# Performance work log

Measured on AMD Instinct MI355X. Metric: run time of the kernel, lower is better.

## Reference

```python
import jax, jax.numpy as jnp
import numpy as np

IN_F = 4096
OUT_F = 4096
B, S = 4, 2048


def _quantize_weight(w_float):
    """Replicates Int4PackedLinear.__init__ double quantization; returns reg_b and w_scale."""
    w_amax = jnp.abs(w_float).max()
    scale = jnp.where(w_amax == 0, 1.0, w_amax / 127.0)
    w_int8 = jnp.clip(jnp.round(w_float / scale), -127, 127).astype(jnp.int8)
    low4_amax = jnp.abs(w_int8.astype(jnp.float32)).max()
    low4_scale = jnp.where(low4_amax == 0, 1.0, low4_amax / 7.0)
    w_low = jnp.clip(jnp.round(w_int8.astype(jnp.float32) / low4_scale), -7, 7).astype(jnp.int8)
    w_rec = jnp.round(w_low.astype(jnp.float32) * low4_scale).astype(jnp.int8)
    w_high = jnp.clip(w_int8.astype(jnp.int32) - w_rec.astype(jnp.int32), -7, 7).astype(jnp.int8)
    reg_b = (w_rec.astype(jnp.int32) + w_high.astype(jnp.int32)).astype(jnp.int8)  # w_combined
    return reg_b, scale.astype(jnp.float32)


def setup_inputs() -> dict:
    key = jax.random.key(0)
    k1, k2, k3 = jax.random.split(key, 3)
    w_float = jax.random.normal(k1, (OUT_F, IN_F), dtype=jnp.float32) * 0.02
    reg_b, w_scale = _quantize_weight(w_float)
    x = jax.random.normal(k2, (B, S, IN_F), dtype=jnp.float32)
    bias = jax.random.normal(k3, (OUT_F,), dtype=jnp.float32) * 0.01
    # gate=1.0 >= threshold=0.3 -> full-precision INT8 path uses reg_b
    return {"x": x, "w_int": reg_b, "w_scale": w_scale, "bias": bias}


def reference(x, w_int, w_scale, bias):
    # --- dynamic per-tensor activation quantization ---
    x_amax = jnp.abs(x).max()
    x_scale = jnp.where(x_amax == 0, jnp.float32(1.0), x_amax / 127.0)
    x_int8 = jnp.clip(jnp.round(x / x_scale), -127, 127).astype(jnp.int8)
    # --- integer matmul (accumulate in int32, like torch._int_mm) ---
    out_i32 = jnp.einsum(
        'bsk,nk->bsn',
        x_int8.astype(jnp.int32),
        w_int.astype(jnp.int32),
    )  # [B, S, OUT_F]
    # --- dequant scale in bf16 AFTER the integer matmul, then bias add ---
    combined_scale = (x_scale * w_scale).astype(jnp.bfloat16)
    out = out_i32.astype(jnp.bfloat16) * combined_scale
    out = out + bias  # bf16 + fp32 -> fp32, matching torch promotion
    return out
```

## Files before the change

kernel.cpp:

```cpp
#include <hip/hip_runtime.h>
#include <hip/hip_bf16.h>
#include <stdint.h>

#define IN_F  4096
#define OUT_F 4096
#define BSZ   4
#define SEQ   2048
#define MDIM  (BSZ * SEQ)

typedef __attribute__((address_space(1))) uint8_t ga_u8_t;
typedef __attribute__((address_space(3))) uint8_t ls_u8_t;

__device__ __forceinline__ void gload16_lds(const void* g, void* l) {
    __builtin_amdgcn_global_load_lds((ga_u8_t*)g, (ls_u8_t*)l, 16, 0, 0);
}

__device__ __forceinline__ float bf16_rne(float f) {
    unsigned u = __float_as_uint(f);
    u = (u + 0x7fffu + ((u >> 16) & 1u)) & 0xffff0000u;
    return __uint_as_float(u);
}

__global__ void amax_kernel(const float* __restrict__ x, int n4,
                            unsigned int* __restrict__ amax_u) {
    const float4* x4 = (const float4*)x;
    int idx = blockIdx.x * blockDim.x + threadIdx.x;
    int stride = gridDim.x * blockDim.x;
    float m = 0.0f;
    for (int i = idx; i < n4; i += stride) {
        float4 v = x4[i];
        m = fmaxf(m, fmaxf(fmaxf(fabsf(v.x), fabsf(v.y)),
                           fmaxf(fabsf(v.z), fabsf(v.w))));
    }
    for (int off = 32; off > 0; off >>= 1)
        m = fmaxf(m, __shfl_down(m, off, 64));
    __shared__ float sm[4];
    int lane = threadIdx.x & 63, wave = threadIdx.x >> 6;
    if (lane == 0) sm[wave] = m;
    __syncthreads();
    if (threadIdx.x == 0) {
        m = fmaxf(fmaxf(sm[0], sm[1]), fmaxf(sm[2], sm[3]));
        atomicMax(amax_u, __float_as_uint(m));
    }
}

__global__ void quant_kernel(const float* __restrict__ x,
                             signed char* __restrict__ x8,
                             const unsigned int* __restrict__ amax_u, int n4) {
    float amax = __uint_as_float(*amax_u);
    float xs = (amax == 0.0f) ? 1.0f : (amax / 127.0f);
    int idx = blockIdx.x * blockDim.x + threadIdx.x;
    if (idx < n4) {
        float4 v = ((const float4*)x)[idx];
        char4 q;
        q.x = (signed char)fminf(fmaxf(rintf(v.x / xs), -127.0f), 127.0f);
        q.y = (signed char)fminf(fmaxf(rintf(v.y / xs), -127.0f), 127.0f);
        q.z = (signed char)fminf(fmaxf(rintf(v.z / xs), -127.0f), 127.0f);
        q.w = (signed char)fminf(fmaxf(rintf(v.w / xs), -127.0f), 127.0f);
        ((char4*)x8)[idx] = q;
    }
}

__global__ void convw_kernel(const int* __restrict__ w,
                             signed char* __restrict__ w8, int n4) {
    int idx = blockIdx.x * blockDim.x + threadIdx.x;
    if (idx < n4) {
        int4 v = ((const int4*)w)[idx];
        char4 q;
        q.x = (signed char)v.x; q.y = (signed char)v.y;
        q.z = (signed char)v.z; q.w = (signed char)v.w;
        ((char4*)w8)[idx] = q;
    }
}

__global__ __launch_bounds__(256, 2) void gemm_i8_kernel(
    const signed char* __restrict__ A,
    const signed char* __restrict__ B,
    const unsigned int* __restrict__ amax_u,
    const float* __restrict__ wscale_p,
    const float* __restrict__ bias,
    float* __restrict__ out) {
    __shared__ signed char sA[128 * 64];
    __shared__ signed char sB[128 * 64];

    const int t = threadIdx.x;
    const int lane = t & 63;
    const int wave = t >> 6;
    const int wm = wave >> 1;
    const int wn = wave & 1;
    const int tileM = blockIdx.y * 128;
    const int tileN = blockIdx.x * 128;

    const int g0 = t, g1 = t + 256;
    const int ar0 = g0 >> 2, ac0 = ((g0 & 3) ^ ((ar0 >> 1) & 3)) * 16;
    const int ar1 = g1 >> 2, ac1 = ((g1 & 3) ^ ((ar1 >> 1) & 3)) * 16;

    const signed char* gA0 = A + (size_t)(tileM + ar0) * IN_F + ac0;
    const signed char* gA1 = A + (size_t)(tileM + ar1) * IN_F + ac1;
    const signed char* gB0 = B + (size_t)(tileN + ar0) * IN_F + ac0;
    const signed char* gB1 = B + (size_t)(tileN + ar1) * IN_F + ac1;

    signed char* lA0 = sA + g0 * 16;
    signed char* lA1 = sA + g1 * 16;
    signed char* lB0 = sB + g0 * 16;
    signed char* lB1 = sB + g1 * 16;

    using i32x4 = __attribute__((ext_vector_type(4))) int;
    i32x4 acc[4][4] = {};

    const signed char* aptr[4];
    const signed char* bptr[4];
#pragma unroll
    for (int i = 0; i < 4; ++i) {
        int rowa = wm * 64 + i * 16 + (lane & 15);
        int ca = ((lane >> 4) ^ ((rowa >> 1) & 3)) * 16;
        aptr[i] = sA + rowa * 64 + ca;
        int rowb = wn * 64 + i * 16 + (lane & 15);
        int cb = ((lane >> 4) ^ ((rowb >> 1) & 3)) * 16;
        bptr[i] = sB + rowb * 64 + cb;
    }

    for (int k0 = 0; k0 < IN_F; k0 += 64) {
        __syncthreads();
        gload16_lds(gA0 + k0, lA0);
        gload16_lds(gA1 + k0, lA1);
        gload16_lds(gB0 + k0, lB0);
        gload16_lds(gB1 + k0, lB1);
        __syncthreads();

        i32x4 aF[4], bF[4];
#pragma unroll
        for (int i = 0; i < 4; ++i) aF[i] = *(const i32x4*)aptr[i];
#pragma unroll
        for (int j = 0; j < 4; ++j) bF[j] = *(const i32x4*)bptr[j];
#pragma unroll
        for (int i = 0; i < 4; ++i)
#pragma unroll
            for (int j = 0; j < 4; ++j)
                acc[i][j] = __builtin_amdgcn_mfma_i32_16x16x64_i8(
                    aF[i], bF[j], acc[i][j], 0, 0, 0);
    }

    float amax = __uint_as_float(*amax_u);
    float xs = (amax == 0.0f) ? 1.0f : (amax / 127.0f);
    float cs = bf16_rne(xs * wscale_p[0]);

#pragma unroll
    for (int j = 0; j < 4; ++j) {
        int n = tileN + wn * 64 + j * 16 + (lane & 15);
        float bz = bias[n];
#pragma unroll
        for (int i = 0; i < 4; ++i) {
            int row0 = tileM + wm * 64 + i * 16 + (lane >> 4) * 4;
#pragma unroll
            for (int r = 0; r < 4; ++r) {
                float v = bf16_rne((float)acc[i][j][r]);
                float p = bf16_rne(v * cs);
                out[(size_t)(row0 + r) * OUT_F + n] = p + bz;
            }
        }
    }
}

extern "C" void kernel_launch(void* const* d_in, const int* in_sizes, int n_in,
                              void* d_out, int out_size, void* d_ws,
                              size_t ws_size, hipStream_t stream) {
    const float* x = (const float*)d_in[0];
    const int* w_int = (const int*)d_in[1];
    const float* w_scale = (const float*)d_in[2];
    const float* bias = (const float*)d_in[3];
    float* out = (float*)d_out;

    unsigned char* ws = (unsigned char*)d_ws;
    unsigned int* amax_u = (unsigned int*)ws;
    signed char* w8 = (signed char*)(ws + 64);
    signed char* x8 = (signed char*)(ws + 64 + (size_t)OUT_F * IN_F);

    hipMemsetAsync(amax_u, 0, 4, stream);

    const int n_x = MDIM * IN_F;
    const int n_w = OUT_F * IN_F;

    amax_kernel<<<4096, 256, 0, stream>>>(x, n_x / 4, amax_u);
    quant_kernel<<<(n_x / 4) / 256, 256, 0, stream>>>(x, x8, amax_u, n_x / 4);
    convw_kernel<<<(n_w / 4) / 256, 256, 0, stream>>>(w_int, w8, n_w / 4);

    dim3 grid(OUT_F / 128, MDIM / 128);
    gemm_i8_kernel<<<grid, 256, 0, stream>>>(x8, w8, amax_u, w_scale, bias, out);
}
```

Baseline: 472.6 us.

## Use 32x32x32 int8 MFMA with 128-wide K tiles and fuse prep kernels

Switches the GEMM inner loop from 16x16x64 to 32x32x32 int8 MFMA instructions. The K tile doubles to 128, with a new LDS layout that groups 16-byte chunks by K-slice, and launch bounds rise to 4 blocks per CU. The activation-quantize and weight-convert kernels are merged into one launch to save a kernel launch. The new LDS layout drops the XOR swizzle, so it may cause bank conflicts, and the larger LDS tiles may limit the occupancy target.

```diff
diff --git a/kernel.cpp b/kernel.cpp
--- a/kernel.cpp
+++ b/kernel.cpp
@@ -44,13 +44,16 @@
     }
 }
 
-__global__ void quant_kernel(const float* __restrict__ x,
-                             signed char* __restrict__ x8,
-                             const unsigned int* __restrict__ amax_u, int n4) {
-    float amax = __uint_as_float(*amax_u);
-    float xs = (amax == 0.0f) ? 1.0f : (amax / 127.0f);
+__global__ void prep_kernel(const float* __restrict__ x,
+                            const int* __restrict__ w,
+                            signed char* __restrict__ x8,
+                            signed char* __restrict__ w8,
+                            const unsigned int* __restrict__ amax_u,
+                            int nx4, int nw4) {
     int idx = blockIdx.x * blockDim.x + threadIdx.x;
-    if (idx < n4) {
+    if (idx < nx4) {
+        float amax = __uint_as_float(*amax_u);
+        float xs = (amax == 0.0f) ? 1.0f : (amax / 127.0f);
         float4 v = ((const float4*)x)[idx];
         char4 q;
         q.x = (signed char)fminf(fmaxf(rintf(v.x / xs), -127.0f), 127.0f);
@@ -58,30 +61,30 @@
         q.z = (signed char)fminf(fmaxf(rintf(v.z / xs), -127.0f), 127.0f);
         q.w = (signed char)fminf(fmaxf(rintf(v.w / xs), -127.0f), 127.0f);
         ((char4*)x8)[idx] = q;
+    } else {
+        int widx = idx - nx4;
+        if (widx < nw4) {
+            int4 v = ((const int4*)w)[widx];
+            char4 q;
+            q.x = (signed char)v.x; q.y = (signed char)v.y;
+            q.z = (signed char)v.z; q.w = (signed char)v.w;
+            ((char4*)w8)[widx] = q;
+        }
     }
 }
 
-__global__ void convw_kernel(const int* __restrict__ w,
-                             signed char* __restrict__ w8, int n4) {
-    int idx = blockIdx.x * blockDim.x + threadIdx.x;
-    if (idx < n4) {
-        int4 v = ((const int4*)w)[idx];
-        char4 q;
-        q.x = (signed char)v.x; q.y = (signed char)v.y;
-        q.z = (signed char)v.z; q.w = (signed char)v.w;
-        ((char4*)w8)[idx] = q;
-    }
-}
+using i32x4 = __attribute__((ext_vector_type(4))) int;
+using i32x16 = __attribute__((ext_vector_type(16))) int;
 
-__global__ __launch_bounds__(256, 2) void gemm_i8_kernel(
+__global__ __launch_bounds__(256, 4) void gemm_i8_kernel(
     const signed char* __restrict__ A,
     const signed char* __restrict__ B,
     const unsigned int* __restrict__ amax_u,
     const float* __restrict__ wscale_p,
     const float* __restrict__ bias,
     float* __restrict__ out) {
-    __shared__ signed char sA[128 * 64];
-    __shared__ signed char sB[128 * 64];
+    __shared__ signed char sA[128 * 128];
+    __shared__ signed char sB[128 * 128];
 
     const int t = threadIdx.x;
     const int lane = t & 63;
@@ -91,54 +94,54 @@
     const int tileM = blockIdx.y * 128;
     const int tileN = blockIdx.x * 128;
 
-    const int g0 = t, g1 = t + 256;
-    const int ar0 = g0 >> 2, ac0 = ((g0 & 3) ^ ((ar0 >> 1) & 3)) * 16;
-    const int ar1 = g1 >> 2, ac1 = ((g1 & 3) ^ ((ar1 >> 1) & 3)) * 16;
-
-    const signed char* gA0 = A + (size_t)(tileM + ar0) * IN_F + ac0;
-    const signed char* gA1 = A + (size_t)(tileM + ar1) * IN_F + ac1;
-    const signed char* gB0 = B + (size_t)(tileN + ar0) * IN_F + ac0;
-    const signed char* gB1 = B + (size_t)(tileN + ar1) * IN_F + ac1;
-
-    signed char* lA0 = sA + g0 * 16;
-    signed char* lA1 = sA + g1 * 16;
-    signed char* lB0 = sB + g0 * 16;
-    signed char* lB1 = sB + g1 * 16;
-
-    using i32x4 = __attribute__((ext_vector_type(4))) int;
-    i32x4 acc[4][4] = {};
-
-    const signed char* aptr[4];
-    const signed char* bptr[4];
+    const signed char* gA[4];
+    const signed char* gB[4];
+    signed char* lA[4];
+    signed char* lB[4];
 #pragma unroll
-    for (int i = 0; i < 4; ++i) {
-        int rowa = wm * 64 + i * 16 + (lane & 15);
-        int ca = ((lane >> 4) ^ ((rowa >> 1) & 3)) * 16;
-        aptr[i] = sA + rowa * 64 + ca;
-        int rowb = wn * 64 + i * 16 + (lane & 15);
-        int cb = ((lane >> 4) ^ ((rowb >> 1) & 3)) * 16;
-        bptr[i] = sB + rowb * 64 + cb;
+    for (int s = 0; s < 4; ++s) {
+        int G = t + 256 * s;
+        int row = G & 127, ch = G >> 7;
+        gA[s] = A + (size_t)(tileM + row) * IN_F + ch * 16;
+        gB[s] = B + (size_t)(tileN + row) * IN_F + ch * 16;
+        lA[s] = sA + G * 16;
+        lB[s] = sB + G * 16;
     }
 
-    for (int k0 = 0; k0 < IN_F; k0 += 64) {
+    int aoff[2], boff[2];
+#pragma unroll
+    for (int i = 0; i < 2; ++i) {
+        aoff[i] = (((lane >> 5) * 128) + wm * 64 + i * 32 + (lane & 31)) * 16;
+        boff[i] = (((lane >> 5) * 128) + wn * 64 + i * 32 + (lane & 31)) * 16;
+    }
+
+    i32x16 acc[2][2] = {};
+
+    for (int k0 = 0; k0 < IN_F; k0 += 128) {
         __syncthreads();
-        gload16_lds(gA0 + k0, lA0);
-        gload16_lds(gA1 + k0, lA1);
-        gload16_lds(gB0 + k0, lB0);
-        gload16_lds(gB1 + k0, lB1);
+#pragma unroll
+        for (int s = 0; s < 4; ++s) {
+            gload16_lds(gA[s] + k0, lA[s]);
+            gload16_lds(gB[s] + k0, lB[s]);
+        }
         __syncthreads();
 
-        i32x4 aF[4], bF[4];
 #pragma unroll
-        for (int i = 0; i < 4; ++i) aF[i] = *(const i32x4*)aptr[i];
+        for (int ks = 0; ks < 4; ++ks) {
+            i32x4 aF[2], bF[2];
 #pragma unroll
-        for (int j = 0; j < 4; ++j) bF[j] = *(const i32x4*)bptr[j];
+            for (int i = 0; i < 2; ++i)
+                aF[i] = *(const i32x4*)(sA + ks * 4096 + aoff[i]);
 #pragma unroll
-        for (int i = 0; i < 4; ++i)
+            for (int j = 0; j < 2; ++j)
+                bF[j] = *(const i32x4*)(sB + ks * 4096 + boff[j]);
 #pragma unroll
-            for (int j = 0; j < 4; ++j)
-                acc[i][j] = __builtin_amdgcn_mfma_i32_16x16x64_i8(
-                    aF[i], bF[j], acc[i][j], 0, 0, 0);
+            for (int i = 0; i < 2; ++i)
+#pragma unroll
+                for (int j = 0; j < 2; ++j)
+                    acc[i][j] = __builtin_amdgcn_mfma_i32_32x32x32_i8(
+                        aF[i], bF[j], acc[i][j], 0, 0, 0);
+        }
     }
 
     float amax = __uint_as_float(*amax_u);
@@ -146,17 +149,18 @@
     float cs = bf16_rne(xs * wscale_p[0]);
 
 #pragma unroll
-    for (int j = 0; j < 4; ++j) {
-        int n = tileN + wn * 64 + j * 16 + (lane & 15);
+    for (int j = 0; j < 2; ++j) {
+        int n = tileN + wn * 64 + j * 32 + (lane & 31);
         float bz = bias[n];
 #pragma unroll
-        for (int i = 0; i < 4; ++i) {
-            int row0 = tileM + wm * 64 + i * 16 + (lane >> 4) * 4;
+        for (int i = 0; i < 2; ++i) {
+            int rbase = tileM + wm * 64 + i * 32 + 4 * (lane >> 5);
 #pragma unroll
-            for (int r = 0; r < 4; ++r) {
+            for (int r = 0; r < 16; ++r) {
+                int row = rbase + (r & 3) + 8 * (r >> 2);
                 float v = bf16_rne((float)acc[i][j][r]);
                 float p = bf16_rne(v * cs);
-                out[(size_t)(row0 + r) * OUT_F + n] = p + bz;
+                out[(size_t)row * OUT_F + n] = p + bz;
             }
         }
     }
@@ -178,12 +182,12 @@
 
     hipMemsetAsync(amax_u, 0, 4, stream);
 
-    const int n_x = MDIM * IN_F;
-    const int n_w = OUT_F * IN_F;
+    const int n_x4 = MDIM * IN_F / 4;
+    const int n_w4 = OUT_F * IN_F / 4;
 
-    amax_kernel<<<4096, 256, 0, stream>>>(x, n_x / 4, amax_u);
-    quant_kernel<<<(n_x / 4) / 256, 256, 0, stream>>>(x, x8, amax_u, n_x / 4);
-    convw_kernel<<<(n_w / 4) / 256, 256, 0, stream>>>(w_int, w8, n_w / 4);
+    amax_kernel<<<4096, 256, 0, stream>>>(x, n_x4, amax_u);
+    prep_kernel<<<(n_x4 + n_w4) / 256, 256, 0, stream>>>(
+        x, w_int, x8, w8, amax_u, n_x4, n_w4);
 
     dim3 grid(OUT_F / 128, MDIM / 128);
     gemm_i8_kernel<<<grid, 256, 0, stream>>>(x8, w8, amax_u, w_scale, bias, out);
```

After: 591.8 us. +25.2%, slower.
